# Kernel tuning notes

Hardware: AMD Instinct MI355X
Metric: run time of the kernel (lower is better)

## Reference

```python
import jax, jax.numpy as jnp
import numpy as np

N_NODES = 100000
N_EDGES = 1600000
N_GRAPHS = 100
DIMS = [128, 128, 118, 103, 5]  # in_feats, h, h-10, h-25, num_classes


def setup_inputs() -> dict:
    key = jax.random.key(0)
    ks = jax.random.split(key, 16)
    inp = {
        "in_feat": jax.random.normal(ks[0], (N_NODES, DIMS[0]), dtype=jnp.float32),
        "src": jax.random.randint(ks[1], (N_EDGES,), 0, N_NODES, dtype=jnp.int32),
        "dst": jax.random.randint(ks[2], (N_EDGES,), 0, N_NODES, dtype=jnp.int32),
        "graph_ids": (jnp.arange(N_NODES, dtype=jnp.int32) // (N_NODES // N_GRAPHS)),
    }
    # SAGEConv params: fc_self (no bias), fc_neigh (no bias), shared bias
    for l in range(4):
        din, dout = DIMS[l], DIMS[l + 1]
        inp[f"ws{l+1}"] = jax.random.normal(ks[3 + 3 * l], (din, dout), dtype=jnp.float32) * 0.05
        inp[f"wn{l+1}"] = jax.random.normal(ks[4 + 3 * l], (din, dout), dtype=jnp.float32) * 0.05
        inp[f"b{l+1}"] = jnp.zeros((dout,), dtype=jnp.float32)
    return inp


def reference(in_feat, src, dst, graph_ids,
              ws1, wn1, b1, ws2, wn2, b2, ws3, wn3, b3, ws4, wn4, b4):
    N = in_feat.shape[0]
    # in-degree per dst node, clamped to 1 (DGL: degs.clamp(min=1))
    deg = jnp.clip(jax.ops.segment_sum(jnp.ones((src.shape[0],), in_feat.dtype), dst,
                                       num_segments=N), 1.0, None)

    def sage(h, ws, wn, b):
        # mean-aggregate neighbor features: gather over src, scatter-add to dst
        agg = jax.ops.segment_sum(h[src], dst, num_segments=N) / deg[:, None]
        return h @ ws + agg @ wn + b

    h = jax.nn.relu(sage(in_feat, ws1, wn1, b1))
    h = jax.nn.relu(sage(h, ws2, wn2, b2))
    h = jax.nn.relu(sage(h, ws3, wn3, b3))
    h = sage(h, ws4, wn4, b4)

    # dgl.mean_nodes: per-graph mean pooling over nodes
    ones = jnp.ones((N,), h.dtype)
    cnt = jax.ops.segment_sum(ones, graph_ids, num_segments=N_GRAPHS)
    pooled = jax.ops.segment_sum(h, graph_ids, num_segments=N_GRAPHS) / cnt[:, None]
    return pooled
```

## Files before the change

kernel.cpp:

```cpp
#include <hip/hip_runtime.h>
#include <cstdint>
#include <cstddef>

typedef unsigned int uint32;
typedef unsigned short ushort16;
typedef __attribute__((ext_vector_type(8))) short short8;
typedef __attribute__((ext_vector_type(4))) float floatx4;

__device__ __forceinline__ ushort16 f2bf(float f) {
    uint32 u = __builtin_bit_cast(uint32, f);
    uint32 r = (u + 0x7fffu + ((u >> 16) & 1u)) >> 16;
    return (ushort16)r;
}
__device__ __forceinline__ float bf2f(ushort16 h) {
    uint32 u = ((uint32)h) << 16;
    return __builtin_bit_cast(float, u);
}

__global__ void hist_kernel(const int* __restrict__ idx, int* __restrict__ cnt, int n) {
    int i = blockIdx.x * blockDim.x + threadIdx.x;
    if (i < n) atomicAdd(&cnt[idx[i]], 1);
}

__global__ void scan_local_kernel(const int* __restrict__ in, int* __restrict__ out,
                                  int* __restrict__ blockSums, int n) {
    __shared__ int sh[256];
    int t = threadIdx.x, b = blockIdx.x;
    int base = b * 1024 + t * 4;
    int v0 = 0, v1 = 0, v2 = 0, v3 = 0;
    if (base + 0 < n) v0 = in[base + 0];
    if (base + 1 < n) v1 = in[base + 1];
    if (base + 2 < n) v2 = in[base + 2];
    if (base + 3 < n) v3 = in[base + 3];
    int s = v0 + v1 + v2 + v3;
    sh[t] = s;
    __syncthreads();
    for (int off = 1; off < 256; off <<= 1) {
        int x = (t >= off) ? sh[t - off] : 0;
        __syncthreads();
        sh[t] += x;
        __syncthreads();
    }
    int excl = sh[t] - s;
    if (t == 255) blockSums[b] = sh[255];
    if (base + 0 < n) out[base + 0] = excl; excl += v0;
    if (base + 1 < n) out[base + 1] = excl; excl += v1;
    if (base + 2 < n) out[base + 2] = excl; excl += v2;
    if (base + 3 < n) out[base + 3] = excl;
}

__global__ void scan_blocks_kernel(const int* __restrict__ bs, int* __restrict__ bo, int nb) {
    __shared__ int sh[256];
    int t = threadIdx.x;
    int s = (t < nb) ? bs[t] : 0;
    sh[t] = s;
    __syncthreads();
    for (int off = 1; off < 256; off <<= 1) {
        int x = (t >= off) ? sh[t - off] : 0;
        __syncthreads();
        sh[t] += x;
        __syncthreads();
    }
    if (t < nb) bo[t] = sh[t] - s;
}

__global__ void scan_add_kernel(int* __restrict__ out, const int* __restrict__ bo, int n, int total) {
    int t = threadIdx.x, b = blockIdx.x;
    int add = bo[b];
    int base = b * 1024 + t * 4;
#pragma unroll
    for (int j = 0; j < 4; ++j) {
        int i = base + j;
        if (i < n) out[i] += add;
    }
    if (b == 0 && t == 0) out[n] = total;
}

__global__ void prep_cursors_kernel(const int* __restrict__ row_ptr, const int* __restrict__ deg,
                                    int* __restrict__ cursor2, int* __restrict__ cursorA,
                                    float* __restrict__ degf, int N, int NBUCK) {
    int i = blockIdx.x * blockDim.x + threadIdx.x;
    if (i < N) {
        cursor2[i] = row_ptr[i];
        int d = deg[i];
        degf[i] = (float)(d > 0 ? d : 1);
    }
    if (i < NBUCK) cursorA[i] = row_ptr[i << 8];
}

#define PBS 4096
__global__ __launch_bounds__(256) void bucket_partition_kernel(
    const int* __restrict__ src, const int* __restrict__ dst,
    int* __restrict__ cursorA, uint32* __restrict__ ebuf, int E, int NBUCK) {
    __shared__ int lbase[512];
    int tid = threadIdx.x;
    for (int b = tid; b < NBUCK; b += 256) lbase[b] = 0;
    __syncthreads();
    int e0 = blockIdx.x * PBS;
    int e1 = e0 + PBS; if (e1 > E) e1 = E;
    for (int j = e0 + tid; j < e1; j += 256)
        atomicAdd(&lbase[dst[j] >> 8], 1);
    __syncthreads();
    for (int b = tid; b < NBUCK; b += 256) {
        int c = lbase[b];
        lbase[b] = c ? atomicAdd(&cursorA[b], c) : 0;
    }
    __syncthreads();
    for (int j = e0 + tid; j < e1; j += 256) {
        int d = dst[j];
        int p = atomicAdd(&lbase[d >> 8], 1);
        ebuf[p] = ((uint32)src[j] << 8) | (uint32)(d & 255);
    }
}

__global__ __launch_bounds__(256) void bucket_fill_kernel(
    const uint32* __restrict__ ebuf, const int* __restrict__ row_ptr,
    int* __restrict__ cursor2, int* __restrict__ csr, int N) {
    int b = blockIdx.x;
    int n0 = b << 8;
    int n1 = n0 + 256; if (n1 > N) n1 = N;
    int s = row_ptr[n0], e = row_ptr[n1];
    for (int j = s + threadIdx.x; j < e; j += 256) {
        uint32 v = ebuf[j];
        int d = n0 | (int)(v & 255u);
        int p = atomicAdd(&cursor2[d], 1);
        csr[p] = (int)(v >> 8);
    }
}

__global__ void conv_bf16_kernel(const float* __restrict__ x, ushort16* __restrict__ y, int n8) {
    int i = blockIdx.x * blockDim.x + threadIdx.x;
    if (i >= n8) return;
    const float4 a = *(const float4*)(x + (size_t)i * 8);
    const float4 b = *(const float4*)(x + (size_t)i * 8 + 4);
    uint4 o;
    o.x = (uint32)f2bf(a.x) | ((uint32)f2bf(a.y) << 16);
    o.y = (uint32)f2bf(a.z) | ((uint32)f2bf(a.w) << 16);
    o.z = (uint32)f2bf(b.x) | ((uint32)f2bf(b.y) << 16);
    o.w = (uint32)f2bf(b.z) | ((uint32)f2bf(b.w) << 16);
    *(uint4*)(y + (size_t)i * 8) = o;
}

__global__ void prep_w_all_kernel(
    const float* __restrict__ W0s, const float* __restrict__ W0n,
    const float* __restrict__ W1s, const float* __restrict__ W1n,
    const float* __restrict__ W2s, const float* __restrict__ W2n,
    ushort16* __restrict__ Whi, ushort16* __restrict__ Wlo) {
    int mat = blockIdx.x >> 6;
    int idx = (blockIdx.x & 63) * 256 + threadIdx.x;
    const float* Wt[6] = {W0s, W0n, W1s, W1n, W2s, W2n};
    const int Kt[6] = {128, 128, 128, 128, 118, 118};
    const int Mt[6] = {128, 128, 118, 118, 103, 103};
    int n = idx >> 7, k = idx & 127;
    int K = Kt[mat], M = Mt[mat];
    float w = (k < K && n < M) ? Wt[mat][(size_t)k * M + n] : 0.f;
    ushort16 h = f2bf(w);
    float lo = w - bf2f(h);
    Whi[(size_t)mat * 16384 + idx] = h;
    Wlo[(size_t)mat * 16384 + idx] = f2bf(lo);
}

template<int UNROLL>
__global__ __launch_bounds__(256) void aggregate_pre_kernel(
    const ushort16* __restrict__ h,
    const int* __restrict__ row_ptr, const int* __restrict__ csr,
    const float* __restrict__ degf, ushort16* __restrict__ aggH, int N) {
    int wid = threadIdx.x >> 6;
    int lane = threadIdx.x & 63;
    int node = blockIdx.x * 4 + wid;
    if (node >= N) return;
    int s = row_ptr[node], e = row_ptr[node + 1];
    int c = lane & 15;
    int eo = lane >> 4;
    float aLo[4] = {}, aHi[4] = {};
    int j = s + eo;
    for (; j + (UNROLL - 1) * 4 < e; j += UNROLL * 4) {
        uint4 v[UNROLL];
#pragma unroll
        for (int u = 0; u < UNROLL; ++u) {
            int src_n = csr[j + u * 4];
            v[u] = *(const uint4*)(h + ((size_t)src_n << 7) + (c << 3));
        }
#pragma unroll
        for (int u = 0; u < UNROLL; ++u) {
            uint32 w[4] = {v[u].x, v[u].y, v[u].z, v[u].w};
#pragma unroll
            for (int p = 0; p < 4; ++p) {
                aLo[p] += __builtin_bit_cast(float, w[p] << 16);
                aHi[p] += __builtin_bit_cast(float, w[p] & 0xffff0000u);
            }
        }
    }
    for (; j < e; j += 4) {
        int src_n = csr[j];
        uint4 v = *(const uint4*)(h + ((size_t)src_n << 7) + (c << 3));
        uint32 w[4] = {v.x, v.y, v.z, v.w};
#pragma unroll
        for (int p = 0; p < 4; ++p) {
            aLo[p] += __builtin_bit_cast(float, w[p] << 16);
            aHi[p] += __builtin_bit_cast(float, w[p] & 0xffff0000u);
        }
    }
#pragma unroll
    for (int m = 16; m < 64; m <<= 1) {
#pragma unroll
        for (int p = 0; p < 4; ++p) {
            aLo[p] += __shfl_xor(aLo[p], m, 64);
            aHi[p] += __shfl_xor(aHi[p], m, 64);
        }
    }
    if (lane < 16) {
        float inv = 1.f / degf[node];
        uint4 ov;
        ov.x = (uint32)f2bf(aLo[0] * inv) | ((uint32)f2bf(aHi[0] * inv) << 16);
        ov.y = (uint32)f2bf(aLo[1] * inv) | ((uint32)f2bf(aHi[1] * inv) << 16);
        ov.z = (uint32)f2bf(aLo[2] * inv) | ((uint32)f2bf(aHi[2] * inv) << 16);
        ov.w = (uint32)f2bf(aLo[3] * inv) | ((uint32)f2bf(aHi[3] * inv) << 16);
        *(uint4*)(aggH + ((size_t)node << 7) + (c << 3)) = ov;
    }
}

#define RS 40
__global__ __launch_bounds__(256) void mfma_fused_kernel(
    const ushort16* __restrict__ A, const ushort16* __restrict__ G,
    const ushort16* __restrict__ Whi, const ushort16* __restrict__ Wlo,
    const float* __restrict__ bias,
    ushort16* __restrict__ Out, int N, int M) {
    __shared__ ushort16 Bs[4][128 * RS];
    const int tid = threadIdx.x;
    const int wave = tid >> 6;
    const int lane = tid & 63;
    const int quad = lane >> 4;
    const int m16 = lane & 15;
    const ushort16* Wg[4] = {Whi, Wlo, Whi + 16384, Wlo + 16384};

    floatx4 acc[8] = {};

    int rowA = blockIdx.x * 64 + wave * 16 + m16;
    if (rowA >= N) rowA = N - 1;
    const ushort16* Arow = A + (size_t)rowA * 128;
    const ushort16* Grow = G + (size_t)rowA * 128;

    const int sn = tid >> 1, shalf = tid & 1;
    for (int k0 = 0; k0 < 128; k0 += 32) {
#pragma unroll
        for (int mat = 0; mat < 4; ++mat) {
            const ushort16* g = Wg[mat] + (size_t)sn * 128 + k0 + shalf * 16;
            uint4 v0 = *(const uint4*)(g);
            uint4 v1 = *(const uint4*)(g + 8);
            ushort16* d = &Bs[mat][sn * RS + shalf * 16];
            *(uint4*)(d) = v0;
            *(uint4*)(d + 8) = v1;
        }
        __syncthreads();
        short8 af = *(const short8*)(Arow + k0 + quad * 8);
        short8 gf = *(const short8*)(Grow + k0 + quad * 8);
#pragma unroll
        for (int t = 0; t < 8; ++t) {
            int nb = t * 16 + m16;
            short8 bsh = *(const short8*)(&Bs[0][nb * RS + quad * 8]);
            short8 bsl = *(const short8*)(&Bs[1][nb * RS + quad * 8]);
            short8 bnh = *(const short8*)(&Bs[2][nb * RS + quad * 8]);
            short8 bnl = *(const short8*)(&Bs[3][nb * RS + quad * 8]);
            acc[t] = __builtin_amdgcn_mfma_f32_16x16x32_bf16(af, bsh, acc[t], 0, 0, 0);
            acc[t] = __builtin_amdgcn_mfma_f32_16x16x32_bf16(gf, bnh, acc[t], 0, 0, 0);
            acc[t] = __builtin_amdgcn_mfma_f32_16x16x32_bf16(af, bsl, acc[t], 0, 0, 0);
            acc[t] = __builtin_amdgcn_mfma_f32_16x16x32_bf16(gf, bnl, acc[t], 0, 0, 0);
        }
        __syncthreads();
    }

    int rowBase = blockIdx.x * 64 + wave * 16 + quad * 4;
#pragma unroll
    for (int t = 0; t < 8; ++t) {
        int col = t * 16 + m16;
        bool inc = (col < M);
        float b = inc ? bias[col] : 0.f;
#pragma unroll
        for (int r = 0; r < 4; ++r) {
            int row = rowBase + r;
            if (row >= N) continue;
            float v = inc ? fmaxf(acc[t][r] + b, 0.f) : 0.f;
            Out[(size_t)row * 128 + col] = f2bf(v);
        }
    }
}

__global__ __launch_bounds__(256) void gemm4_kernel(
    const ushort16* __restrict__ A, const float* __restrict__ ws,
    const float* __restrict__ wn, const float* __restrict__ b4,
    float* __restrict__ Cs, float* __restrict__ Cn, int N, int K, int M) {
    __shared__ float Wsh[520], Wnh[520];
    int tid = threadIdx.x;
    for (int i = tid; i < K * M; i += 256) { Wsh[i] = ws[i]; Wnh[i] = wn[i]; }
    __syncthreads();
    int node = blockIdx.x * 256 + tid;
    if (node >= N) return;
    const ushort16* row = A + ((size_t)node << 7);
    float s[5] = {}, n[5] = {};
    for (int c8 = 0; c8 * 8 < K; ++c8) {
        uint4 v = *(const uint4*)(row + c8 * 8);
        uint32 w[4] = {v.x, v.y, v.z, v.w};
#pragma unroll
        for (int j = 0; j < 8; ++j) {
            int k = c8 * 8 + j;
            if (k < K) {
                float a = (j & 1) ? __builtin_bit_cast(float, w[j >> 1] & 0xffff0000u)
                                  : __builtin_bit_cast(float, w[j >> 1] << 16);
#pragma unroll
                for (int m = 0; m < 5; ++m) {
                    s[m] += a * Wsh[k * 5 + m];
                    n[m] += a * Wnh[k * 5 + m];
                }
            }
        }
    }
    size_t o = (size_t)node * 8;
#pragma unroll
    for (int m = 0; m < 5; ++m) {
        Cs[o + m] = s[m] + b4[m];
        Cn[o + m] = n[m];
    }
#pragma unroll
    for (int m = 5; m < 8; ++m) { Cs[o + m] = 0.f; Cn[o + m] = 0.f; }
}

template<int CPW, int UNROLL, int SLOG>
__global__ __launch_bounds__(256) void aggregate_fp32_kernel(
    const float* __restrict__ hs, const float* __restrict__ hn,
    const int* __restrict__ row_ptr, const int* __restrict__ csr,
    const float* __restrict__ degf, float* __restrict__ out, int N) {
    constexpr int EPI = 64 / CPW;
    int wid = threadIdx.x >> 6;
    int lane = threadIdx.x & 63;
    int node = blockIdx.x * 4 + wid;
    if (node >= N) return;
    int s = row_ptr[node], e = row_ptr[node + 1];
    int c = lane & (CPW - 1);
    int eo = lane / CPW;
    float4 acc = make_float4(0.f, 0.f, 0.f, 0.f);
    int j = s + eo;
    for (; j + (UNROLL - 1) * EPI < e; j += UNROLL * EPI) {
        float4 v[UNROLL];
#pragma unroll
        for (int u = 0; u < UNROLL; ++u) {
            int src_n = csr[j + u * EPI];
            v[u] = *(const float4*)(hn + ((size_t)src_n << SLOG) + (c << 2));
        }
#pragma unroll
        for (int u = 0; u < UNROLL; ++u) {
            acc.x += v[u].x; acc.y += v[u].y; acc.z += v[u].z; acc.w += v[u].w;
        }
    }
    for (; j < e; j += EPI) {
        int src_n = csr[j];
        float4 v = *(const float4*)(hn + ((size_t)src_n << SLOG) + (c << 2));
        acc.x += v.x; acc.y += v.y; acc.z += v.z; acc.w += v.w;
    }
#pragma unroll
    for (int m = CPW; m < 64; m <<= 1) {
        acc.x += __shfl_xor(acc.x, m, 64);
        acc.y += __shfl_xor(acc.y, m, 64);
        acc.z += __shfl_xor(acc.z, m, 64);
        acc.w += __shfl_xor(acc.w, m, 64);
    }
    if (lane < CPW) {
        float d = 1.f / degf[node];
        size_t o = ((size_t)node << SLOG) + (lane << 2);
        float4 hv = *(const float4*)(hs + o);
        float4 r;
        r.x = hv.x + acc.x * d;
        r.y = hv.y + acc.y * d;
        r.z = hv.z + acc.z * d;
        r.w = hv.w + acc.w * d;
        *(float4*)(out + o) = r;
    }
}

__global__ __launch_bounds__(256) void pool_kernel(
    const float* __restrict__ h, float* __restrict__ out, int npg) {
    __shared__ float sh[4][5];
    int g = blockIdx.x;
    int t = threadIdx.x;
    float acc[5] = {0.f, 0.f, 0.f, 0.f, 0.f};
    int base = g * npg;
    for (int i = t; i < npg; i += 256) {
        const float* r = h + ((size_t)(base + i) << 3);
#pragma unroll
        for (int f = 0; f < 5; ++f) acc[f] += r[f];
    }
#pragma unroll
    for (int off = 32; off > 0; off >>= 1) {
#pragma unroll
        for (int f = 0; f < 5; ++f) acc[f] += __shfl_down(acc[f], off, 64);
    }
    int wid = t >> 6, lane = t & 63;
    if (lane == 0) {
#pragma unroll
        for (int f = 0; f < 5; ++f) sh[wid][f] = acc[f];
    }
    __syncthreads();
    if (t == 0) {
        float inv = 1.f / (float)npg;
#pragma unroll
        for (int f = 0; f < 5; ++f)
            out[g * 5 + f] = (sh[0][f] + sh[1][f] + sh[2][f] + sh[3][f]) * inv;
    }
}

extern "C" void kernel_launch(void* const* d_in, const int* in_sizes, int n_in,
                              void* d_out, int out_size, void* d_ws, size_t ws_size,
                              hipStream_t stream) {
    const float* in_feat = (const float*)d_in[0];
    const int* src = (const int*)d_in[1];
    const int* dst = (const int*)d_in[2];
    const int DIMS[5] = {128, 128, 118, 103, 5};
    const int N = in_sizes[0] / 128;
    const int E = in_sizes[1];
    const int G = out_size / 5;
    const int NBUCK = (N + 255) >> 8;

    char* base = (char*)d_ws;
    size_t off = 0;
    auto carve = [&](size_t bytes) -> void* {
        off = (off + 255) & ~(size_t)255;
        void* p = base + off;
        off += bytes;
        return p;
    };
    int* deg_i = (int*)carve((size_t)N * 4);
    float* degf = (float*)carve((size_t)N * 4);
    int* row_ptr = (int*)carve((size_t)(N + 1) * 4);
    int* cursor2 = (int*)carve((size_t)N * 4);
    int* cursorA = (int*)carve((size_t)NBUCK * 4);
    int* blockSums = (int*)carve(256 * 4);
    int* blockOff = (int*)carve(256 * 4);
    uint32* ebuf = (uint32*)carve((size_t)E * 4);
    int* csr = (int*)carve((size_t)E * 4);
    ushort16* buf0 = (ushort16*)carve((size_t)(N + 64) * 128 * 2);
    ushort16* buf1 = (ushort16*)carve((size_t)(N + 64) * 128 * 2);
    ushort16* aggH = (ushort16*)carve((size_t)(N + 64) * 128 * 2);
    ushort16* Whi = (ushort16*)carve((size_t)6 * 16384 * 2);
    ushort16* Wlo = (ushort16*)carve((size_t)6 * 16384 * 2);
    float* Cs4 = (float*)carve((size_t)N * 8 * 4);
    float* Cn4 = (float*)carve((size_t)N * 8 * 4);
    float* out4 = (float*)carve((size_t)N * 8 * 4);
    (void)n_in; (void)ws_size;

    hipMemsetAsync(deg_i, 0, (size_t)N * 4, stream);
    hist_kernel<<<(E + 255) / 256, 256, 0, stream>>>(dst, deg_i, E);
    int nb = (N + 1023) / 1024;
    scan_local_kernel<<<nb, 256, 0, stream>>>(deg_i, row_ptr, blockSums, N);
    scan_blocks_kernel<<<1, 256, 0, stream>>>(blockSums, blockOff, nb);
    scan_add_kernel<<<nb, 256, 0, stream>>>(row_ptr, blockOff, N, E);
    prep_cursors_kernel<<<(N + 255) / 256, 256, 0, stream>>>(
        row_ptr, deg_i, cursor2, cursorA, degf, N, NBUCK);
    bucket_partition_kernel<<<(E + PBS - 1) / PBS, 256, 0, stream>>>(
        src, dst, cursorA, ebuf, E, NBUCK);
    bucket_fill_kernel<<<NBUCK, 256, 0, stream>>>(ebuf, row_ptr, cursor2, csr, N);

    int n8 = N * 16;
    conv_bf16_kernel<<<(n8 + 255) / 256, 256, 0, stream>>>(in_feat, buf0, n8);
    prep_w_all_kernel<<<6 * 64, 256, 0, stream>>>(
        (const float*)d_in[4], (const float*)d_in[5],
        (const float*)d_in[7], (const float*)d_in[8],
        (const float*)d_in[10], (const float*)d_in[11],
        Whi, Wlo);

    ushort16* hb[4] = {buf0, buf1, buf0, buf1};
    int gblocks = (N + 63) / 64;
    for (int l = 0; l < 3; ++l) {
        int M = DIMS[l + 1];
        const float* b = (const float*)d_in[6 + 3 * l];
        aggregate_pre_kernel<4><<<(N + 3) / 4, 256, 0, stream>>>(
            hb[l], row_ptr, csr, degf, aggH, N);
        mfma_fused_kernel<<<gblocks, 256, 0, stream>>>(
            hb[l], aggH, Whi + (size_t)l * 2 * 16384, Wlo + (size_t)l * 2 * 16384,
            b, hb[l + 1], N, M);
    }

    gemm4_kernel<<<(N + 255) / 256, 256, 0, stream>>>(
        hb[3], (const float*)d_in[13], (const float*)d_in[14], (const float*)d_in[15],
        Cs4, Cn4, N, DIMS[3], DIMS[4]);
    aggregate_fp32_kernel<2, 1, 3><<<(N + 3) / 4, 256, 0, stream>>>(
        Cs4, Cn4, row_ptr, csr, degf, out4, N);
    pool_kernel<<<G, 256, 0, stream>>>(out4, (float*)d_out, N / G);
}
```

Baseline: 600.3 us.

## Build CSR via bucket histogram and per-bucket local degree scan

Replaces the global per-node degree histogram (1.6M global atomics onto 100k counters) and its multi-kernel scan with a coarse per-bucket histogram built in shared memory, a single-block bucket scan, and a per-bucket build kernel. The build kernel computes node degrees, row pointers and degf in shared memory and scatters CSR entries with LDS atomics instead of global cursor atomics. This cuts several launches and most global atomic traffic in the graph preprocessing, at the cost of reading ebuf twice per bucket and assuming at most 512 buckets.

Result: faster. 520.2 us (-13.3%).

```diff
diff --git a/kernel.cpp b/kernel.cpp
--- a/kernel.cpp
+++ b/kernel.cpp
@@ -17,78 +17,53 @@
     return __builtin_bit_cast(float, u);
 }
 
-__global__ void hist_kernel(const int* __restrict__ idx, int* __restrict__ cnt, int n) {
-    int i = blockIdx.x * blockDim.x + threadIdx.x;
-    if (i < n) atomicAdd(&cnt[idx[i]], 1);
-}
-
-__global__ void scan_local_kernel(const int* __restrict__ in, int* __restrict__ out,
-                                  int* __restrict__ blockSums, int n) {
-    __shared__ int sh[256];
-    int t = threadIdx.x, b = blockIdx.x;
-    int base = b * 1024 + t * 4;
-    int v0 = 0, v1 = 0, v2 = 0, v3 = 0;
-    if (base + 0 < n) v0 = in[base + 0];
-    if (base + 1 < n) v1 = in[base + 1];
-    if (base + 2 < n) v2 = in[base + 2];
-    if (base + 3 < n) v3 = in[base + 3];
-    int s = v0 + v1 + v2 + v3;
-    sh[t] = s;
-    __syncthreads();
-    for (int off = 1; off < 256; off <<= 1) {
-        int x = (t >= off) ? sh[t - off] : 0;
+#define PBS 4096
+
+
+__global__ __launch_bounds__(256) void bucket_hist_kernel(
+    const int* __restrict__ dst, int* __restrict__ bcnt, int E, int NBUCK) {
+    __shared__ int l[512];
+    int t = threadIdx.x;
+    for (int b = t; b < NBUCK; b += 256) l[b] = 0;
+    __syncthreads();
+    int e0 = blockIdx.x * PBS;
+    int e1 = e0 + PBS; if (e1 > E) e1 = E;
+    for (int j = e0 + t; j < e1; j += 256)
+        atomicAdd(&l[dst[j] >> 8], 1);
+    __syncthreads();
+    for (int b = t; b < NBUCK; b += 256) {
+        int c = l[b];
+        if (c) atomicAdd(&bcnt[b], c);
+    }
+}
+
+__global__ __launch_bounds__(256) void bucket_scan_kernel(
+    const int* __restrict__ bcnt, int* __restrict__ bucketOff,
+    int* __restrict__ cursorA, int NBUCK, int E) {
+    __shared__ int a[512], b[512];
+    int t = threadIdx.x;
+    a[t] = (t < NBUCK) ? bcnt[t] : 0;
+    a[t + 256] = (t + 256 < NBUCK) ? bcnt[t + 256] : 0;
+    __syncthreads();
+    int* cur = a; int* nxt = b;
+    for (int o = 1; o < 512; o <<= 1) {
+#pragma unroll
+        for (int i = t; i < 512; i += 256)
+            nxt[i] = cur[i] + ((i >= o) ? cur[i - o] : 0);
         __syncthreads();
-        sh[t] += x;
-        __syncthreads();
-    }
-    int excl = sh[t] - s;
-    if (t == 255) blockSums[b] = sh[255];
-    if (base + 0 < n) out[base + 0] = excl; excl += v0;
-    if (base + 1 < n) out[base + 1] = excl; excl += v1;
-    if (base + 2 < n) out[base + 2] = excl; excl += v2;
-    if (base + 3 < n) out[base + 3] = excl;
-}
-
-__global__ void scan_blocks_kernel(const int* __restrict__ bs, int* __restrict__ bo, int nb) {
-    __shared__ int sh[256];
-    int t = threadIdx.x;
-    int s = (t < nb) ? bs[t] : 0;
-    sh[t] = s;
-    __syncthreads();
-    for (int off = 1; off < 256; off <<= 1) {
-        int x = (t >= off) ? sh[t - off] : 0;
-        __syncthreads();
-        sh[t] += x;
-        __syncthreads();
-    }
-    if (t < nb) bo[t] = sh[t] - s;
-}
-
-__global__ void scan_add_kernel(int* __restrict__ out, const int* __restrict__ bo, int n, int total) {
-    int t = threadIdx.x, b = blockIdx.x;
-    int add = bo[b];
-    int base = b * 1024 + t * 4;
-#pragma unroll
-    for (int j = 0; j < 4; ++j) {
-        int i = base + j;
-        if (i < n) out[i] += add;
-    }
-    if (b == 0 && t == 0) out[n] = total;
-}
-
-__global__ void prep_cursors_kernel(const int* __restrict__ row_ptr, const int* __restrict__ deg,
-                                    int* __restrict__ cursor2, int* __restrict__ cursorA,
-                                    float* __restrict__ degf, int N, int NBUCK) {
-    int i = blockIdx.x * blockDim.x + threadIdx.x;
-    if (i < N) {
-        cursor2[i] = row_ptr[i];
-        int d = deg[i];
-        degf[i] = (float)(d > 0 ? d : 1);
-    }
-    if (i < NBUCK) cursorA[i] = row_ptr[i << 8];
-}
-
-#define PBS 4096
+        int* tmp = cur; cur = nxt; nxt = tmp;
+    }
+#pragma unroll
+    for (int i = t; i < 512; i += 256) {
+        if (i <= NBUCK) {
+            int off = (i == 0) ? 0 : cur[i - 1];
+            bucketOff[i] = off;
+            if (i < NBUCK) cursorA[i] = off;
+        }
+    }
+    if (t == 0) bucketOff[NBUCK] = E;
+}
+
 __global__ __launch_bounds__(256) void bucket_partition_kernel(
     const int* __restrict__ src, const int* __restrict__ dst,
     int* __restrict__ cursorA, uint32* __restrict__ ebuf, int E, int NBUCK) {
@@ -113,19 +88,44 @@
     }
 }
 
-__global__ __launch_bounds__(256) void bucket_fill_kernel(
-    const uint32* __restrict__ ebuf, const int* __restrict__ row_ptr,
-    int* __restrict__ cursor2, int* __restrict__ csr, int N) {
-    int b = blockIdx.x;
+__global__ __launch_bounds__(256) void bucket_build_kernel(
+    const uint32* __restrict__ ebuf, const int* __restrict__ bucketOff,
+    int* __restrict__ row_ptr, float* __restrict__ degf,
+    int* __restrict__ csr, int N, int E) {
+    __shared__ int ldeg[256];
+    __shared__ int lscan[256];
+    __shared__ int lcur[256];
+    int b = blockIdx.x, t = threadIdx.x;
     int n0 = b << 8;
-    int n1 = n0 + 256; if (n1 > N) n1 = N;
-    int s = row_ptr[n0], e = row_ptr[n1];
-    for (int j = s + threadIdx.x; j < e; j += 256) {
-        uint32 v = ebuf[j];
-        int d = n0 | (int)(v & 255u);
-        int p = atomicAdd(&cursor2[d], 1);
-        csr[p] = (int)(v >> 8);
-    }
+    int s = bucketOff[b], e = bucketOff[b + 1];
+    ldeg[t] = 0;
+    __syncthreads();
+    for (int j = s + t; j < e; j += 256)
+        atomicAdd(&ldeg[ebuf[j] & 255u], 1);
+    __syncthreads();
+    int v = ldeg[t];
+    lscan[t] = v;
+    __syncthreads();
+    for (int off = 1; off < 256; off <<= 1) {
+        int x = (t >= off) ? lscan[t - off] : 0;
+        __syncthreads();
+        lscan[t] += x;
+        __syncthreads();
+    }
+    int excl = lscan[t] - v;
+    int node = n0 + t;
+    if (node < N) {
+        row_ptr[node] = s + excl;
+        degf[node] = (float)(v > 0 ? v : 1);
+    }
+    lcur[t] = s + excl;
+    __syncthreads();
+    for (int j = s + t; j < e; j += 256) {
+        uint32 en = ebuf[j];
+        int p = atomicAdd(&lcur[en & 255u], 1);
+        csr[p] = (int)(en >> 8);
+    }
+    if (b == 0 && t == 0) row_ptr[N] = E;
 }
 
 __global__ void conv_bf16_kernel(const float* __restrict__ x, ushort16* __restrict__ y, int n8) {
@@ -428,13 +428,11 @@
         off += bytes;
         return p;
     };
-    int* deg_i = (int*)carve((size_t)N * 4);
+    int* bcnt = (int*)carve((size_t)NBUCK * 4);
+    int* bucketOff = (int*)carve((size_t)(NBUCK + 1) * 4);
+    int* cursorA = (int*)carve((size_t)NBUCK * 4);
+    int* row_ptr = (int*)carve((size_t)(N + 1) * 4);
     float* degf = (float*)carve((size_t)N * 4);
-    int* row_ptr = (int*)carve((size_t)(N + 1) * 4);
-    int* cursor2 = (int*)carve((size_t)N * 4);
-    int* cursorA = (int*)carve((size_t)NBUCK * 4);
-    int* blockSums = (int*)carve(256 * 4);
-    int* blockOff = (int*)carve(256 * 4);
     uint32* ebuf = (uint32*)carve((size_t)E * 4);
     int* csr = (int*)carve((size_t)E * 4);
     ushort16* buf0 = (ushort16*)carve((size_t)(N + 64) * 128 * 2);
@@ -447,17 +445,13 @@
     float* out4 = (float*)carve((size_t)N * 8 * 4);
     (void)n_in; (void)ws_size;
 
-    hipMemsetAsync(deg_i, 0, (size_t)N * 4, stream);
-    hist_kernel<<<(E + 255) / 256, 256, 0, stream>>>(dst, deg_i, E);
-    int nb = (N + 1023) / 1024;
-    scan_local_kernel<<<nb, 256, 0, stream>>>(deg_i, row_ptr, blockSums, N);
-    scan_blocks_kernel<<<1, 256, 0, stream>>>(blockSums, blockOff, nb);
-    scan_add_kernel<<<nb, 256, 0, stream>>>(row_ptr, blockOff, N, E);
-    prep_cursors_kernel<<<(N + 255) / 256, 256, 0, stream>>>(
-        row_ptr, deg_i, cursor2, cursorA, degf, N, NBUCK);
+    hipMemsetAsync(bcnt, 0, (size_t)NBUCK * 4, stream);
+    bucket_hist_kernel<<<(E + PBS - 1) / PBS, 256, 0, stream>>>(dst, bcnt, E, NBUCK);
+    bucket_scan_kernel<<<1, 256, 0, stream>>>(bcnt, bucketOff, cursorA, NBUCK, E);
     bucket_partition_kernel<<<(E + PBS - 1) / PBS, 256, 0, stream>>>(
         src, dst, cursorA, ebuf, E, NBUCK);
-    bucket_fill_kernel<<<NBUCK, 256, 0, stream>>>(ebuf, row_ptr, cursor2, csr, N);
+    bucket_build_kernel<<<NBUCK, 256, 0, stream>>>(
+        ebuf, bucketOff, row_ptr, degf, csr, N, E);
 
     int n8 = N * 16;
     conv_bf16_kernel<<<(n8 + 255) / 256, 256, 0, stream>>>(in_feat, buf0, n8);
```
